# Optimization experiments

Hardware: AMD Instinct MI355X
Metric: run time of the kernel (lower is better)

## Reference

```python
import jax, jax.numpy as jnp
import numpy as np

DIM = 512  # DIM_IMAGE_EMBEDDING
HEAD = 64
B, T = 16, 2048


def setup_inputs() -> dict:
    key = jax.random.key(0)
    ks = jax.random.split(key, 8)
    s = 1.0 / np.sqrt(DIM)
    return {
        'x': jax.random.normal(ks[0], (B, T, DIM), jnp.float32),
        'Wq': jax.random.normal(ks[1], (HEAD, DIM), jnp.float32) * s,
        'Wk': jax.random.normal(ks[2], (HEAD, DIM), jnp.float32) * s,
        'Wv': jax.random.normal(ks[3], (HEAD, DIM), jnp.float32) * s,
        'fx_real': jax.random.normal(ks[4], (T, HEAD // 4), jnp.float32),
        'fx_imag': jax.random.normal(ks[5], (T, HEAD // 4), jnp.float32),
        'fy_real': jax.random.normal(ks[6], (T, HEAD // 4), jnp.float32),
        'fy_imag': jax.random.normal(ks[7], (T, HEAD // 4), jnp.float32),
    }


def _rotate_half(t, fr, fi):
    # t: [B, T, H/2] viewed as H/4 complex pairs; fr, fi: [T, H/4]
    b, s, d = t.shape
    tc = t.reshape(b, s, d // 2, 2)
    a, bb = tc[..., 0], tc[..., 1]
    ro = a * fr - bb * fi  # real part of complex product
    io = a * fi + bb * fr  # imag part
    return jnp.stack([ro, io], axis=-1).reshape(b, s, d)


def apply_rotary_2d(t, fx_real, fx_imag, fy_real, fy_imag):
    h = t.shape[-1] // 2
    vx = _rotate_half(t[..., :h], fx_real, fx_imag)
    vy = _rotate_half(t[..., h:], fy_real, fy_imag)
    return jnp.concatenate([vx, vy], axis=-1)


def reference(x, Wq, Wk, Wv, fx_real, fx_imag, fy_real, fy_imag):
    C = x.shape[-1]
    q = jnp.einsum('btc,hc->bth', x, Wq)
    k = jnp.einsum('btc,hc->bth', x, Wk)
    v = jnp.einsum('btc,hc->bth', x, Wv)
    q = apply_rotary_2d(q, fx_real, fx_imag, fy_real, fy_imag)
    k = apply_rotary_2d(k, fx_real, fx_imag, fy_real, fy_imag)
    # NOTE: original scales by input dim C (=512), not head_size
    wei = jnp.einsum('bqh,bkh->bqk', q, k) / jnp.sqrt(jnp.float32(C))
    softwei = jax.nn.softmax(wei, axis=-1)
    out = jnp.einsum('bqk,bkh->bqh', softwei, v)
    return out
```

## Files before the change

### kernel.cpp

```cpp
#include <hip/hip_runtime.h>
#include <hip/hip_bf16.h>

#define BB 16
#define TT 2048
#define DIMC 512
#define HEADH 64

typedef __attribute__((ext_vector_type(8))) short short8v;
typedef __attribute__((ext_vector_type(4))) float f32x4;

static __device__ __forceinline__ unsigned short f2bf(float f) {
    __hip_bfloat16 h = __float2bfloat16(f);
    unsigned short u;
    __builtin_memcpy(&u, &h, 2);
    return u;
}
static __device__ __forceinline__ unsigned int packbf(float lo, float hi) {
    float2 f2; f2.x = lo; f2.y = hi;
    __hip_bfloat162 h2 = __float22bfloat162_rn(f2);
    unsigned int u;
    __builtin_memcpy(&u, &h2, 4);
    return u;
}
#define EXP2R __builtin_amdgcn_exp2f
static __device__ __forceinline__ void async_copy16(void* lds, const void* g) {
    __builtin_amdgcn_global_load_lds(
        (const __attribute__((address_space(1))) unsigned char*)g,
        (__attribute__((address_space(3))) unsigned char*)lds, 16, 0, 0);
}

union bfrag {
    unsigned int u[4];
    short8v v;
};

__global__ __launch_bounds__(256) void wcvt_kernel(
    const float* __restrict__ Wq, const float* __restrict__ Wk,
    const float* __restrict__ Wv, unsigned short* __restrict__ wb)
{
    const int idx = blockIdx.x * 256 + threadIdx.x;
    const int e   = idx << 3;
    const int row = e >> 9, col = e & 511;
    const float* src = (row < 64) ? Wq : (row < 128) ? Wk : Wv;
    const float* p = src + (size_t)(row & 63) * DIMC + col;
    float4 a = *(const float4*)p;
    float4 b = *(const float4*)(p + 4);
    uint4 o;
    o.x = packbf(a.x, a.y); o.y = packbf(a.z, a.w);
    o.z = packbf(b.x, b.y); o.w = packbf(b.z, b.w);
    *(uint4*)(wb + e) = o;
}

__global__ __launch_bounds__(256, 2) void qkv_mfma_kernel(
    const float* __restrict__ x,
    const unsigned short* __restrict__ wb,
    const float* __restrict__ fxr, const float* __restrict__ fxi,
    const float* __restrict__ fyr, const float* __restrict__ fyi,
    unsigned short* __restrict__ qo, unsigned short* __restrict__ ko,
    unsigned short* __restrict__ vt)
{
    __shared__ unsigned char xlds[16384];

    const int tid = threadIdx.x;
    const int w   = tid >> 6;
    const int l   = tid & 63;
    const int q   = l & 15;
    const int g   = l >> 4;
    const int t0  = blockIdx.x << 6;

    f32x4 acc[3][4];
    #pragma unroll
    for (int j = 0; j < 3; ++j)
        #pragma unroll
        for (int tt = 0; tt < 4; ++tt) acc[j][tt] = (f32x4){0.f, 0.f, 0.f, 0.f};

    const unsigned short* wp0 = wb + ((size_t)((3 * w + 0) * 16 + q)) * DIMC + 8 * g;
    const unsigned short* wp1 = wb + ((size_t)((3 * w + 1) * 16 + q)) * DIMC + 8 * g;
    const unsigned short* wp2 = wb + ((size_t)((3 * w + 2) * 16 + q)) * DIMC + 8 * g;

    const int rl = l >> 3;
    const int cb = (l & 7) ^ rl;
    const float* xsrc0 = x + (size_t)(t0 + 16 * w + 0 + rl) * DIMC + 4 * cb;
    const float* xsrc1 = x + (size_t)(t0 + 16 * w + 8 + rl) * DIMC + 4 * cb;
    unsigned char* xdst0 = xlds + (16 * w + 0) * 128;
    unsigned char* xdst1 = xlds + (16 * w + 8) * 128;

#define STAGE_X(bufsel, k0) do {                                              \
        async_copy16(xdst0 + (bufsel) * 8192, xsrc0 + (k0));                  \
        async_copy16(xdst1 + (bufsel) * 8192, xsrc1 + (k0));                  \
    } while (0)

    STAGE_X(0, 0);
    __syncthreads();

    int cur = 0;
    for (int it = 0; it < 16; ++it) {
        const int k0 = it << 5;
        if (it < 15) STAGE_X(cur ^ 1, k0 + 32);

        short8v wf0 = *(const short8v*)(wp0 + k0);
        short8v wf1 = *(const short8v*)(wp1 + k0);
        short8v wf2 = *(const short8v*)(wp2 + k0);

        const unsigned char* xb = xlds + cur * 8192;
        #pragma unroll
        for (int tt = 0; tt < 4; ++tt) {
            const int rr = tt * 16 + q;
            const int s0 = (2 * g)     ^ (q & 7);
            const int s1 = (2 * g + 1) ^ (q & 7);
            float4 f0 = *(const float4*)(xb + rr * 128 + s0 * 16);
            float4 f1 = *(const float4*)(xb + rr * 128 + s1 * 16);
            bfrag xv;
            xv.u[0] = packbf(f0.x, f0.y); xv.u[1] = packbf(f0.z, f0.w);
            xv.u[2] = packbf(f1.x, f1.y); xv.u[3] = packbf(f1.z, f1.w);
            acc[0][tt] = __builtin_amdgcn_mfma_f32_16x16x32_bf16(wf0, xv.v, acc[0][tt], 0, 0, 0);
            acc[1][tt] = __builtin_amdgcn_mfma_f32_16x16x32_bf16(wf1, xv.v, acc[1][tt], 0, 0, 0);
            acc[2][tt] = __builtin_amdgcn_mfma_f32_16x16x32_bf16(wf2, xv.v, acc[2][tt], 0, 0, 0);
        }

        __syncthreads();
        cur ^= 1;
    }

    const float qscale = 1.4426950408889634f / 22.627416997969522f;
    #pragma unroll
    for (int j = 0; j < 3; ++j) {
        const int gt   = 3 * w + j;
        const int mat  = gt >> 2;
        const int hbase = (gt & 3) * 16 + 4 * g;
        #pragma unroll
        for (int tt = 0; tt < 4; ++tt) {
            const int trow = t0 + tt * 16 + q;
            const int tl   = trow & (TT - 1);
            if (mat == 2) {
                const int b = trow >> 11;
                #pragma unroll
                for (int r = 0; r < 4; ++r)
                    vt[((size_t)(b * HEADH) + hbase + r) * TT + tl] = f2bf(acc[j][tt][r]);
            } else {
                const float sc = (mat == 0) ? qscale : 1.f;
                unsigned short* dst = ((mat == 0) ? qo : ko) + (size_t)trow * HEADH;
                const int half = hbase >> 5;
                const float* frt = half ? fyr : fxr;
                const float* fit = half ? fyi : fxi;
                const int pi0 = (hbase & 31) >> 1;
                float fr0 = frt[tl * 16 + pi0],     fi0 = fit[tl * 16 + pi0];
                float fr1 = frt[tl * 16 + pi0 + 1], fi1 = fit[tl * 16 + pi0 + 1];
                float e0 = acc[j][tt][0] * fr0 - acc[j][tt][1] * fi0;
                float e1 = acc[j][tt][0] * fi0 + acc[j][tt][1] * fr0;
                float e2 = acc[j][tt][2] * fr1 - acc[j][tt][3] * fi1;
                float e3 = acc[j][tt][2] * fi1 + acc[j][tt][3] * fr1;
                uint2 ow;
                ow.x = packbf(e0 * sc, e1 * sc);
                ow.y = packbf(e2 * sc, e3 * sc);
                *(uint2*)(dst + hbase) = ow;
            }
        }
    }
#undef STAGE_X
}

__global__ __launch_bounds__(512, 4) void attn_mfma_kernel(
    const unsigned short* __restrict__ qws,
    const unsigned short* __restrict__ kws,
    const unsigned short* __restrict__ vtw,
    float* __restrict__ out)
{
    __shared__ unsigned char smem[81920];

    const int tid = threadIdx.x;
    const int w   = tid >> 6;
    const int wq  = w & 3;
    const int h   = w >> 2;
    const int l   = tid & 63;
    const int q   = l & 15;
    const int g   = l >> 4;
    const int b   = blockIdx.x >> 5;
    const int q0  = (blockIdx.x & 31) << 6;
    const int qw  = q0 + 16 * wq;
    const int rx  = q & 7;
    const int swz = (q & 7) << 2;

    const int rl = l >> 3;
    const int sl = (l & 7) ^ rl;

    unsigned int* pldsw = (unsigned int*)(smem + 65536 + (w << 11));

    const unsigned short* kbase = kws + (size_t)b * TT * HEADH;
    const unsigned short* vbase = vtw + (size_t)b * HEADH * TT;

    const unsigned short* ksrc0 = kbase + (size_t)(h * 1024 + 16 * wq + rl) * HEADH + 8 * sl;
    const unsigned short* ksrc1 = ksrc0 + (size_t)8 * HEADH;
    const unsigned short* vsrc0 = vbase + (size_t)(16 * wq + rl) * TT + h * 1024 + 8 * sl;
    const unsigned short* vsrc1 = vsrc0 + (size_t)8 * TT;

#define STAGE_TILE(bufsel, kv)  do {                                          \
        unsigned char* kd = smem + (h << 14) + (bufsel) * 8192 + (wq << 11);  \
        async_copy16(kd,        ksrc0 + (size_t)(kv) * HEADH);                \
        async_copy16(kd + 1024, ksrc1 + (size_t)(kv) * HEADH);                \
        unsigned char* vd = smem + 32768 + (h << 14) + (bufsel) * 8192 + (wq << 11); \
        async_copy16(vd,        vsrc0 + (kv));                                \
        async_copy16(vd + 1024, vsrc1 + (kv));                                \
    } while (0)

    short8v qf0, qf1;
    {
        const unsigned short* qp = qws + ((size_t)(b * TT + qw + q)) * HEADH + 8 * g;
        qf0 = *(const short8v*)(qp);
        qf1 = *(const short8v*)(qp + 32);
    }

    f32x4 oacc[4];
    #pragma unroll
    for (int mt = 0; mt < 4; ++mt) oacc[mt] = (f32x4){0.f, 0.f, 0.f, 0.f};
    float m = -1e30f, lsum = 0.f;

    STAGE_TILE(0, 0);
    __syncthreads();

    int cur = 0;
    for (int it = 0; it < 16; ++it) {
        const int kv0 = it << 6;
        if (it < 15) STAGE_TILE(cur ^ 1, kv0 + 64);

        const unsigned char* kb = smem + (h << 14) + cur * 8192;
        const unsigned char* vb = smem + 32768 + (h << 14) + cur * 8192;

        f32x4 sacc[4];
        #pragma unroll
        for (int n = 0; n < 4; ++n) {
            const int r = 16 * n + q;
            const short8v k0 = *(const short8v*)(kb + r * 128 + ((g ^ rx) << 4));
            const short8v k1 = *(const short8v*)(kb + r * 128 + (((4 + g) ^ rx) << 4));
            f32x4 z = (f32x4){0.f, 0.f, 0.f, 0.f};
            z = __builtin_amdgcn_mfma_f32_16x16x32_bf16(k0, qf0, z, 0, 0, 0);
            z = __builtin_amdgcn_mfma_f32_16x16x32_bf16(k1, qf1, z, 0, 0, 0);
            sacc[n] = z;
        }

        float cmax = sacc[0][0];
        #pragma unroll
        for (int n = 0; n < 4; ++n)
            #pragma unroll
            for (int r = 0; r < 4; ++r) cmax = fmaxf(cmax, sacc[n][r]);
        cmax = fmaxf(cmax, __shfl_xor(cmax, 16));
        cmax = fmaxf(cmax, __shfl_xor(cmax, 32));
        const float mnew = fmaxf(m, cmax);

        float p[4][4];
        #pragma unroll
        for (int n = 0; n < 4; ++n) {
            #pragma unroll
            for (int r = 0; r < 4; ++r)
                p[n][r] = EXP2R(sacc[n][r] - mnew);
            uint2 wv;
            wv.x = packbf(p[n][0], p[n][1]);
            wv.y = packbf(p[n][2], p[n][3]);
            *(uint2*)&pldsw[q * 32 + ((8 * n + 2 * g) ^ swz)] = wv;
        }

        const float sc = EXP2R(m - mnew);
        if (__any(cmax > m)) {
            #pragma unroll
            for (int mt = 0; mt < 4; ++mt)
                #pragma unroll
                for (int r = 0; r < 4; ++r) oacc[mt][r] *= sc;
        }

        #pragma unroll
        for (int s = 0; s < 2; ++s) {
            const short8v pb = *(const short8v*)&pldsw[q * 32 + ((16 * s + 4 * g) ^ swz)];
            #pragma unroll
            for (int mt = 0; mt < 4; ++mt) {
                const int d = 16 * mt + q;
                const short8v vfr = *(const short8v*)(vb + d * 128 + ((((s << 2) + g) ^ rx) << 4));
                oacc[mt] = __builtin_amdgcn_mfma_f32_16x16x32_bf16(vfr, pb, oacc[mt], 0, 0, 0);
            }
        }

        float psum = 0.f;
        #pragma unroll
        for (int n = 0; n < 4; ++n)
            #pragma unroll
            for (int r = 0; r < 4; ++r) psum += p[n][r];
        psum += __shfl_xor(psum, 16);
        psum += __shfl_xor(psum, 32);
        lsum = lsum * sc + psum;
        m = mnew;

        __syncthreads();
        cur ^= 1;
    }

    __syncthreads();
    float* o_f  = (float*)smem;
    float* ml_f = (float*)(smem + 32768);
    {
        const int prow = h * 64 + 16 * wq + q;
        #pragma unroll
        for (int mt = 0; mt < 4; ++mt)
            *(f32x4*)&o_f[prow * 64 + 16 * mt + 4 * g] = oacc[mt];
        if (g == 0) {
            ml_f[h * 128 + 16 * wq + q]      = m;
            ml_f[h * 128 + 64 + 16 * wq + q] = lsum;
        }
    }
    __syncthreads();

    const int cq = tid >> 3;
    const int ch = (tid & 7) << 3;
    const float m0 = ml_f[cq],       l0 = ml_f[64 + cq];
    const float m1 = ml_f[128 + cq], l1 = ml_f[192 + cq];
    const float M  = fmaxf(m0, m1);
    const float a0 = EXP2R(m0 - M), a1 = EXP2R(m1 - M);
    const float inv = 1.f / (a0 * l0 + a1 * l1);
    const float* o0 = &o_f[cq * 64 + ch];
    const float* o1 = &o_f[(64 + cq) * 64 + ch];
    float4 A0 = *(const float4*)(o0), B0 = *(const float4*)(o0 + 4);
    float4 A1 = *(const float4*)(o1), B1 = *(const float4*)(o1 + 4);
    float* op = out + ((size_t)(b * TT + q0 + cq)) * HEADH + ch;
    *(float4*)(op)     = make_float4((a0 * A0.x + a1 * A1.x) * inv,
                                     (a0 * A0.y + a1 * A1.y) * inv,
                                     (a0 * A0.z + a1 * A1.z) * inv,
                                     (a0 * A0.w + a1 * A1.w) * inv);
    *(float4*)(op + 4) = make_float4((a0 * B0.x + a1 * B1.x) * inv,
                                     (a0 * B0.y + a1 * B1.y) * inv,
                                     (a0 * B0.z + a1 * B1.z) * inv,
                                     (a0 * B0.w + a1 * B1.w) * inv);
#undef STAGE_TILE
}

extern "C" void kernel_launch(void* const* d_in, const int* in_sizes, int n_in,
                              void* d_out, int out_size, void* d_ws, size_t ws_size,
                              hipStream_t stream)
{
    const float* x   = (const float*)d_in[0];
    const float* Wq  = (const float*)d_in[1];
    const float* Wk  = (const float*)d_in[2];
    const float* Wv  = (const float*)d_in[3];
    const float* fxr = (const float*)d_in[4];
    const float* fxi = (const float*)d_in[5];
    const float* fyr = (const float*)d_in[6];
    const float* fyi = (const float*)d_in[7];
    float* out = (float*)d_out;

    unsigned short* qo = (unsigned short*)d_ws;
    unsigned short* ko = qo + (size_t)BB * TT * HEADH;
    unsigned short* vt = ko + (size_t)BB * TT * HEADH;
    unsigned short* wb = vt + (size_t)BB * TT * HEADH;

    wcvt_kernel<<<48, 256, 0, stream>>>(Wq, Wk, Wv, wb);
    qkv_mfma_kernel<<<(BB * TT) / 64, 256, 0, stream>>>(x, wb, fxr, fxi, fyr, fyi,
                                                        qo, ko, vt);
    attn_mfma_kernel<<<BB * 32, 512, 0, stream>>>(qo, ko, vt, out);
}
```

Measured before the change: 67.86 us.

## Double x staging tile depth in QKV projection and tree-reduce attention row max

The QKV projection kernel now stages 64 columns of x per iteration instead of 32. The LDS buffer grows to 32KB with a 16-way XOR swizzle, which halves the number of loop iterations and barriers. Both main loops get unroll-2 hints. The attention row max becomes a tree reduction, which shortens the dependent fmax chain. The cost is doubled LDS use in the projection kernel, which may reduce occupancy, and more register pressure from unrolling.

```diff
diff --git a/kernel.cpp b/kernel.cpp
--- a/kernel.cpp
+++ b/kernel.cpp
@@ -59,7 +59,7 @@
     unsigned short* __restrict__ qo, unsigned short* __restrict__ ko,
     unsigned short* __restrict__ vt)
 {
-    __shared__ unsigned char xlds[16384];
+    __shared__ unsigned char xlds[32768];
 
     const int tid = threadIdx.x;
     const int w   = tid >> 6;
@@ -78,44 +78,53 @@
     const unsigned short* wp1 = wb + ((size_t)((3 * w + 1) * 16 + q)) * DIMC + 8 * g;
     const unsigned short* wp2 = wb + ((size_t)((3 * w + 2) * 16 + q)) * DIMC + 8 * g;
 
-    const int rl = l >> 3;
-    const int cb = (l & 7) ^ rl;
-    const float* xsrc0 = x + (size_t)(t0 + 16 * w + 0 + rl) * DIMC + 4 * cb;
-    const float* xsrc1 = x + (size_t)(t0 + 16 * w + 8 + rl) * DIMC + 4 * cb;
-    unsigned char* xdst0 = xlds + (16 * w + 0) * 128;
-    unsigned char* xdst1 = xlds + (16 * w + 8) * 128;
+    const int rl4 = l >> 4;
+    const int s16 = l & 15;
+    const float* xsrcc[4];
+    #pragma unroll
+    for (int c = 0; c < 4; ++c) {
+        const int cb = s16 ^ (4 * c + rl4);
+        xsrcc[c] = x + (size_t)(t0 + 16 * w + 4 * c + rl4) * DIMC + 4 * cb;
+    }
+    unsigned char* xdst = xlds + 16 * w * 256;
 
 #define STAGE_X(bufsel, k0) do {                                              \
-        async_copy16(xdst0 + (bufsel) * 8192, xsrc0 + (k0));                  \
-        async_copy16(xdst1 + (bufsel) * 8192, xsrc1 + (k0));                  \
+        unsigned char* d = xdst + (bufsel) * 16384;                           \
+        async_copy16(d,        xsrcc[0] + (k0));                              \
+        async_copy16(d + 1024, xsrcc[1] + (k0));                              \
+        async_copy16(d + 2048, xsrcc[2] + (k0));                              \
+        async_copy16(d + 3072, xsrcc[3] + (k0));                              \
     } while (0)
 
     STAGE_X(0, 0);
     __syncthreads();
 
     int cur = 0;
-    for (int it = 0; it < 16; ++it) {
-        const int k0 = it << 5;
-        if (it < 15) STAGE_X(cur ^ 1, k0 + 32);
-
-        short8v wf0 = *(const short8v*)(wp0 + k0);
-        short8v wf1 = *(const short8v*)(wp1 + k0);
-        short8v wf2 = *(const short8v*)(wp2 + k0);
-
-        const unsigned char* xb = xlds + cur * 8192;
-        #pragma unroll
-        for (int tt = 0; tt < 4; ++tt) {
-            const int rr = tt * 16 + q;
-            const int s0 = (2 * g)     ^ (q & 7);
-            const int s1 = (2 * g + 1) ^ (q & 7);
-            float4 f0 = *(const float4*)(xb + rr * 128 + s0 * 16);
-            float4 f1 = *(const float4*)(xb + rr * 128 + s1 * 16);
-            bfrag xv;
-            xv.u[0] = packbf(f0.x, f0.y); xv.u[1] = packbf(f0.z, f0.w);
-            xv.u[2] = packbf(f1.x, f1.y); xv.u[3] = packbf(f1.z, f1.w);
-            acc[0][tt] = __builtin_amdgcn_mfma_f32_16x16x32_bf16(wf0, xv.v, acc[0][tt], 0, 0, 0);
-            acc[1][tt] = __builtin_amdgcn_mfma_f32_16x16x32_bf16(wf1, xv.v, acc[1][tt], 0, 0, 0);
-            acc[2][tt] = __builtin_amdgcn_mfma_f32_16x16x32_bf16(wf2, xv.v, acc[2][tt], 0, 0, 0);
+    #pragma unroll 2
+    for (int it = 0; it < 8; ++it) {
+        const int k0 = it << 6;
+        if (it < 7) STAGE_X(cur ^ 1, k0 + 64);
+
+        const unsigned char* xb = xlds + cur * 16384;
+        #pragma unroll
+        for (int ks = 0; ks < 2; ++ks) {
+            short8v wf0 = *(const short8v*)(wp0 + k0 + 32 * ks);
+            short8v wf1 = *(const short8v*)(wp1 + k0 + 32 * ks);
+            short8v wf2 = *(const short8v*)(wp2 + k0 + 32 * ks);
+            #pragma unroll
+            for (int tt = 0; tt < 4; ++tt) {
+                const int rr = tt * 16 + q;
+                const int s0 = (8 * ks + 2 * g)     ^ q;
+                const int s1 = (8 * ks + 2 * g + 1) ^ q;
+                float4 f0 = *(const float4*)(xb + rr * 256 + s0 * 16);
+                float4 f1 = *(const float4*)(xb + rr * 256 + s1 * 16);
+                bfrag xv;
+                xv.u[0] = packbf(f0.x, f0.y); xv.u[1] = packbf(f0.z, f0.w);
+                xv.u[2] = packbf(f1.x, f1.y); xv.u[3] = packbf(f1.z, f1.w);
+                acc[0][tt] = __builtin_amdgcn_mfma_f32_16x16x32_bf16(wf0, xv.v, acc[0][tt], 0, 0, 0);
+                acc[1][tt] = __builtin_amdgcn_mfma_f32_16x16x32_bf16(wf1, xv.v, acc[1][tt], 0, 0, 0);
+                acc[2][tt] = __builtin_amdgcn_mfma_f32_16x16x32_bf16(wf2, xv.v, acc[2][tt], 0, 0, 0);
+            }
         }
 
         __syncthreads();
@@ -219,6 +228,7 @@
     __syncthreads();
 
     int cur = 0;
+    #pragma unroll 2
     for (int it = 0; it < 16; ++it) {
         const int kv0 = it << 6;
         if (it < 15) STAGE_TILE(cur ^ 1, kv0 + 64);
@@ -238,11 +248,12 @@
             sacc[n] = z;
         }
 
-        float cmax = sacc[0][0];
+        float nx[4];
         #pragma unroll
         for (int n = 0; n < 4; ++n)
-            #pragma unroll
-            for (int r = 0; r < 4; ++r) cmax = fmaxf(cmax, sacc[n][r]);
+            nx[n] = fmaxf(fmaxf(sacc[n][0], sacc[n][1]),
+                          fmaxf(sacc[n][2], sacc[n][3]));
+        float cmax = fmaxf(fmaxf(nx[0], nx[1]), fmaxf(nx[2], nx[3]));
         cmax = fmaxf(cmax, __shfl_xor(cmax, 16));
         cmax = fmaxf(cmax, __shfl_xor(cmax, 32));
         const float mnew = fmaxf(m, cmax);
```

Result: slower. 70.19 us (+3.4%).
